# Kernel tuning notes

Hardware: AMD Instinct MI355X
Metric: run time of the kernel (lower is better)

The kernel has to match this reference:

```python
import jax, jax.numpy as jnp
import numpy as np

MUL = 32           # multiplicity of each irrep in Rs_in / Rs_out
R_EPS = 0.1        # radius below which the linear fallback kernel is used
SQRT3 = np.float32(np.sqrt(3.0))

# real-basis Levi-Civita = wigner_3j(1,1,1) * sqrt(6)
_EPS3 = np.zeros((3, 3, 3), np.float32)
_EPS3[0, 1, 2] = _EPS3[1, 2, 0] = _EPS3[2, 0, 1] = 1.0
_EPS3[0, 2, 1] = _EPS3[2, 1, 0] = _EPS3[1, 0, 2] = -1.0


def _frozen_kernel(r, W1, b1, W2, b2, lin_w0, lin_w1):
    N = r.shape[0]
    radii = jnp.linalg.norm(r, axis=1)                 # [N]
    mask = radii > R_EPS                               # [N] valid edges
    safe = jnp.where(mask, radii, jnp.ones_like(radii))
    unit = r / safe[:, None]                           # [N,3] safe unit vectors

    # radial MLP R: r -> R^(5*MUL*MUL); computed densely, masked rows replaced below
    h = jax.nn.relu(radii[:, None] * W1 + b1)          # [N,H]
    R = (h @ W2 + b2).reshape(N, 5, MUL, MUL)          # [N, path, w(out), u(in)]
    R0a, R0b, R1a, R1b, R1c = (R[:, i] for i in range(5))

    # component-normalized spherical harmonics: Y0 = 1, Y1 = sqrt(3)*unit
    Y1 = SQRT3 * unit                                  # [N,3]

    # per-path normalization: 1/sqrt(n_paths_into_output * mul_in)
    n0 = np.float32(1.0 / np.sqrt(2 * MUL))            # output l=0: 2 paths
    n1 = np.float32(1.0 / np.sqrt(3 * MUL))            # output l=1: 3 paths
    I3 = jnp.eye(3, dtype=r.dtype)
    eps3 = jnp.asarray(_EPS3, dtype=r.dtype)

    # CG tensor-product kernel blocks (w3j contracted analytically for l<=1)
    K00 = n0 * R0a                                                      # [N,w,u]
    K01 = (n0 / SQRT3) * jnp.einsum('nwu,ni->nwui', R1b, Y1)            # in l=1 -> out l=0
    K10 = n1 * jnp.einsum('nwu,nj->nwju', R1a, Y1)                      # in l=0 -> out l=1
    K11 = n1 * (jnp.einsum('nwu,ji->nwjui', R0b, I3)                    # l_f=0 path
                + np.float32(1.0 / np.sqrt(2.0))
                * jnp.einsum('nwu,nk,ikj->nwjui', R1c, Y1, eps3))       # l_f=1 path

    D = 4 * MUL  # dim = MUL*(1) + MUL*(3)
    kernel1 = jnp.zeros((N, D, D), r.dtype)
    kernel1 = kernel1.at[:, :MUL, :MUL].set(K00)
    kernel1 = kernel1.at[:, :MUL, MUL:].set(K01.reshape(N, MUL, 3 * MUL))
    kernel1 = kernel1.at[:, MUL:, :MUL].set(K10.reshape(N, 3 * MUL, MUL))
    kernel1 = kernel1.at[:, MUL:, MUL:].set(K11.reshape(N, 3 * MUL, 3 * MUL))

    # KernelLinear fallback for radii <= r_eps: block diag per l, scaled 1/sqrt(mul_in)
    s = np.float32(1.0 / np.sqrt(MUL))
    k2_11 = s * jnp.einsum('wu,ji->wjui', lin_w1, I3).reshape(3 * MUL, 3 * MUL)
    kernel2 = jnp.zeros((D, D), r.dtype)
    kernel2 = kernel2.at[:MUL, :MUL].set(s * lin_w0)
    kernel2 = kernel2.at[MUL:, MUL:].set(k2_11)

    return jnp.where(mask[:, None, None], kernel1, kernel2[None, :, :])


def setup_inputs() -> dict:
    key = jax.random.key(0)
    ks = jax.random.split(key, 6)
    N, H = 4000, 128
    r = jax.random.normal(ks[0], (N, 3), jnp.float32)
    r = r.at[:100].multiply(0.01)  # push some radii under r_eps -> fallback path
    W1 = jax.random.normal(ks[1], (1, H), jnp.float32)
    b1 = jnp.zeros((H,), jnp.float32)
    W2 = jax.random.normal(ks[2], (H, 5 * MUL * MUL), jnp.float32) / np.float32(np.sqrt(H))
    b2 = jnp.zeros((5 * MUL * MUL,), jnp.float32)
    lin_w0 = jax.random.normal(ks[3], (MUL, MUL), jnp.float32)
    lin_w1 = jax.random.normal(ks[4], (MUL, MUL), jnp.float32)
    return dict(r=r, W1=W1, b1=b1, W2=W2, b2=b2, lin_w0=lin_w0, lin_w1=lin_w1)


def reference(r, W1, b1, W2, b2, lin_w0, lin_w1):
    return _frozen_kernel(r, W1, b1, W2, b2, lin_w0, lin_w1)
```

## Files before the change

### kernel.cpp

```cpp
#include <hip/hip_runtime.h>
#include <math.h>

#define H 128
#define MUL 32
#define NC (5 * MUL * MUL)
#define DD (4 * MUL)
#define NIV (H + 1)
#define NMAX 4000

__device__ float g_bp[H];
__device__ int   g_nbp;
__device__ float g_rmid[NIV];
__device__ float g_A[NIV * NC];
__device__ float g_B[NIV * NC];
__device__ float4 g_ey[NMAX];
__device__ int    g_eidx[NMAX];

__global__ void prep_bp(const float* __restrict__ W1, const float* __restrict__ b1) {
    __shared__ float bp[H];
    __shared__ float sorted[H];
    int k = threadIdx.x;
    float a = W1[k], b = b1[k];
    float v = 3.0e38f;
    if (a != 0.0f) {
        float t = -b / a;
        if (t > 0.0f) v = t;
    }
    bp[k] = v;
    __syncthreads();
    int rank = 0, nv = 0;
    #pragma unroll 8
    for (int j = 0; j < H; ++j) {
        float bj = bp[j];
        rank += (bj < v) || (bj == v && j < k);
        nv   += (bj < 3.0e38f);
    }
    sorted[rank] = v;
    __syncthreads();
    g_bp[k] = sorted[k];
    if (k == 0) g_nbp = nv;
    int nbp = nv;
    for (int i = k; i <= H; i += H) {
        float rm;
        if (nbp == 0)       rm = 1.0f;
        else if (i == 0)    rm = 0.5f * sorted[0];
        else if (i >= nbp)  rm = sorted[nbp - 1] + 1.0f;
        else                rm = 0.5f * (sorted[i - 1] + sorted[i]);
        g_rmid[i] = rm;
    }
}

__global__ void prep_edges(const float* __restrict__ r, int N) {
    int n = blockIdx.x * blockDim.x + threadIdx.x;
    if (n >= N) return;
    float x = r[3 * n], y = r[3 * n + 1], z = r[3 * n + 2];
    float rad = sqrtf(x * x + y * y + z * z);
    bool mask = rad > 0.1f;
    float inv = mask ? (1.7320508075688772f / rad) : 0.0f;
    g_ey[n] = make_float4(x * inv, y * inv, z * inv, rad);
    int idx = -1;
    if (mask) {
        int nbp = g_nbp;
        idx = 0;
        for (int j = 0; j < nbp; ++j) idx += (g_bp[j] < rad) ? 1 : 0;
    }
    g_eidx[n] = idx;
}

__global__ __launch_bounds__(256) void prep_tab(const float* __restrict__ W1,
                                                const float* __restrict__ b1,
                                                const float* __restrict__ W2,
                                                const float* __restrict__ b2) {
    int i = blockIdx.y;
    if (i > g_nbp) return;
    int c = blockIdx.x * 256 + threadIdx.x;
    float rm = g_rmid[i];
    float accA = 0.0f, accB = 0.0f;
    #pragma unroll 4
    for (int k = 0; k < H; ++k) {
        float a = W1[k], b = b1[k];
        float w2 = W2[k * NC + c];
        bool act = (a * rm + b) > 0.0f;
        accA += act ? a * w2 : 0.0f;
        accB += act ? b * w2 : 0.0f;
    }
    g_A[i * NC + c] = accA;
    g_B[i * NC + c] = accB + b2[c];
}

__global__ __launch_bounds__(256) void main_kernel(const float* __restrict__ lin_w0,
                                                   const float* __restrict__ lin_w1,
                                                   float* __restrict__ out, int N) {
    int bid   = blockIdx.x;
    int wuBlk = bid & 15;
    int eBlk  = bid >> 4;
    int tx = threadIdx.x & 63;
    int tz = threadIdx.x >> 6;
    int n  = eBlk * 4 + tz;
    if (n >= N) return;
    int wu = wuBlk * 64 + tx;
    int w = wu >> 5, u = wu & 31;

    float* o = out + (size_t)n * (DD * DD);
    int row1 = MUL + 3 * w;
    int col1 = MUL + 3 * u;
    int idx = g_eidx[n];

    if (idx >= 0) {
        float4 ey = g_ey[n];
        float rad = ey.w;
        const float* Arow = g_A + (size_t)idx * NC;
        const float* Brow = g_B + (size_t)idx * NC;
        float acc[5];
        #pragma unroll
        for (int p = 0; p < 5; ++p) {
            int c = p * (MUL * MUL) + wu;
            acc[p] = rad * Arow[c] + Brow[c];
        }
        const float n0   = 0.125f;
        const float n1   = 0.10206207261596575f;
        const float n0s3 = 0.07216878364870323f;
        const float n1s2 = 0.07216878364870323f;
        float Y0 = ey.x, Y1 = ey.y, Y2 = ey.z;

        o[w * DD + u] = n0 * acc[0];
        float v3 = n0s3 * acc[3];
        o[w * DD + col1 + 0] = v3 * Y0;
        o[w * DD + col1 + 1] = v3 * Y1;
        o[w * DD + col1 + 2] = v3 * Y2;
        float v2 = n1 * acc[2];
        o[(row1 + 0) * DD + u] = v2 * Y0;
        o[(row1 + 1) * DD + u] = v2 * Y1;
        o[(row1 + 2) * DD + u] = v2 * Y2;
        float d = n1 * acc[1];
        float e = n1s2 * acc[4];
        float eY0 = e * Y0, eY1 = e * Y1, eY2 = e * Y2;
        o[(row1 + 0) * DD + col1 + 0] = d;
        o[(row1 + 0) * DD + col1 + 1] = eY2;
        o[(row1 + 0) * DD + col1 + 2] = -eY1;
        o[(row1 + 1) * DD + col1 + 0] = -eY2;
        o[(row1 + 1) * DD + col1 + 1] = d;
        o[(row1 + 1) * DD + col1 + 2] = eY0;
        o[(row1 + 2) * DD + col1 + 0] = eY1;
        o[(row1 + 2) * DD + col1 + 1] = -eY0;
        o[(row1 + 2) * DD + col1 + 2] = d;
    } else {
        const float s = 0.17677669529663687f;
        float v0 = s * lin_w0[w * MUL + u];
        float v1 = s * lin_w1[w * MUL + u];
        o[w * DD + u] = v0;
        o[w * DD + col1 + 0] = 0.0f;
        o[w * DD + col1 + 1] = 0.0f;
        o[w * DD + col1 + 2] = 0.0f;
        o[(row1 + 0) * DD + u] = 0.0f;
        o[(row1 + 1) * DD + u] = 0.0f;
        o[(row1 + 2) * DD + u] = 0.0f;
        o[(row1 + 0) * DD + col1 + 0] = v1;
        o[(row1 + 0) * DD + col1 + 1] = 0.0f;
        o[(row1 + 0) * DD + col1 + 2] = 0.0f;
        o[(row1 + 1) * DD + col1 + 0] = 0.0f;
        o[(row1 + 1) * DD + col1 + 1] = v1;
        o[(row1 + 1) * DD + col1 + 2] = 0.0f;
        o[(row1 + 2) * DD + col1 + 0] = 0.0f;
        o[(row1 + 2) * DD + col1 + 1] = 0.0f;
        o[(row1 + 2) * DD + col1 + 2] = v1;
    }
}

extern "C" void kernel_launch(void* const* d_in, const int* in_sizes, int n_in,
                              void* d_out, int out_size, void* d_ws, size_t ws_size,
                              hipStream_t stream) {
    const float* r   = (const float*)d_in[0];
    const float* W1  = (const float*)d_in[1];
    const float* b1  = (const float*)d_in[2];
    const float* W2  = (const float*)d_in[3];
    const float* b2  = (const float*)d_in[4];
    const float* lw0 = (const float*)d_in[5];
    const float* lw1 = (const float*)d_in[6];
    float* out = (float*)d_out;
    int N = in_sizes[0] / 3;

    prep_bp<<<dim3(1), dim3(H), 0, stream>>>(W1, b1);
    prep_edges<<<dim3((N + 255) / 256), dim3(256), 0, stream>>>(r, N);
    prep_tab<<<dim3(NC / 256, NIV), dim3(256), 0, stream>>>(W1, b1, W2, b2);
    int eChunks = (N + 3) / 4;
    main_kernel<<<dim3(eChunks * 16), dim3(256), 0, stream>>>(lw0, lw1, out, N);
}
```

Before: 68.23 us.

## Write output rows as coalesced float4 stores with one block per edge

The main kernel now assigns one block per edge and has each thread compute four consecutive output columns, writing them with a single float4 store in row-major order. Previously each thread scattered 16 scalar stores across strided rows and columns. The aim is fully coalesced, wide writes for the 256 MB output. The cost is more index arithmetic and repeated table loads, since A/B entries for the l=1 blocks are re-read for each of the three components.

```diff
diff --git a/kernel.cpp b/kernel.cpp
--- a/kernel.cpp
+++ b/kernel.cpp
@@ -15,6 +15,10 @@
 __device__ float g_B[NIV * NC];
 __device__ float4 g_ey[NMAX];
 __device__ int    g_eidx[NMAX];
+
+__device__ __forceinline__ float sel3(int i, float a, float b, float c) {
+    return (i == 0) ? a : ((i == 1) ? b : c);
+}
 
 __global__ void prep_bp(const float* __restrict__ W1, const float* __restrict__ b1) {
     __shared__ float bp[H];
@@ -91,79 +95,106 @@
 __global__ __launch_bounds__(256) void main_kernel(const float* __restrict__ lin_w0,
                                                    const float* __restrict__ lin_w1,
                                                    float* __restrict__ out, int N) {
-    int bid   = blockIdx.x;
-    int wuBlk = bid & 15;
-    int eBlk  = bid >> 4;
-    int tx = threadIdx.x & 63;
-    int tz = threadIdx.x >> 6;
-    int n  = eBlk * 4 + tz;
+    int n = blockIdx.x;
     if (n >= N) return;
-    int wu = wuBlk * 64 + tx;
-    int w = wu >> 5, u = wu & 31;
-
-    float* o = out + (size_t)n * (DD * DD);
-    int row1 = MUL + 3 * w;
-    int col1 = MUL + 3 * u;
     int idx = g_eidx[n];
+    float4* o4 = reinterpret_cast<float4*>(out + (size_t)n * (DD * DD));
+
+    const float n0   = 0.125f;
+    const float n1   = 0.10206207261596575f;
+    const float ns   = 0.07216878364870323f;
 
     if (idx >= 0) {
         float4 ey = g_ey[n];
+        float Y0 = ey.x, Y1 = ey.y, Y2 = ey.z;
         float rad = ey.w;
-        const float* Arow = g_A + (size_t)idx * NC;
-        const float* Brow = g_B + (size_t)idx * NC;
-        float acc[5];
+        const float* __restrict__ A = g_A + (size_t)idx * NC;
+        const float* __restrict__ B = g_B + (size_t)idx * NC;
+
         #pragma unroll
-        for (int p = 0; p < 5; ++p) {
-            int c = p * (MUL * MUL) + wu;
-            acc[p] = rad * Arow[c] + Brow[c];
+        for (int it = 0; it < 16; ++it) {
+            int pos  = it * 256 + threadIdx.x;
+            int row  = pos >> 5;
+            int col0 = (pos & 31) << 2;
+            float v[4];
+            if (row < MUL) {
+                int w = row;
+                if (col0 < MUL) {
+                    #pragma unroll
+                    for (int q = 0; q < 4; ++q) {
+                        int c = w * MUL + col0 + q;
+                        v[q] = n0 * (rad * A[c] + B[c]);
+                    }
+                } else {
+                    #pragma unroll
+                    for (int q = 0; q < 4; ++q) {
+                        int cc = col0 + q - MUL;
+                        int u  = (cc * 171) >> 9;
+                        int i  = cc - 3 * u;
+                        int c  = 3 * (MUL * MUL) + w * MUL + u;
+                        v[q] = ns * (rad * A[c] + B[c]) * sel3(i, Y0, Y1, Y2);
+                    }
+                }
+            } else {
+                int rr = row - MUL;
+                int w  = (rr * 171) >> 9;
+                int j  = rr - 3 * w;
+                float Yj = sel3(j, Y0, Y1, Y2);
+                int jp = (j == 2) ? 0 : (j + 1);
+                if (col0 < MUL) {
+                    #pragma unroll
+                    for (int q = 0; q < 4; ++q) {
+                        int c = 2 * (MUL * MUL) + w * MUL + col0 + q;
+                        v[q] = n1 * (rad * A[c] + B[c]) * Yj;
+                    }
+                } else {
+                    #pragma unroll
+                    for (int q = 0; q < 4; ++q) {
+                        int cc = col0 + q - MUL;
+                        int u  = (cc * 171) >> 9;
+                        int i  = cc - 3 * u;
+                        int c1 = 1 * (MUL * MUL) + w * MUL + u;
+                        int c4 = 4 * (MUL * MUL) + w * MUL + u;
+                        float rb = rad * A[c1] + B[c1];
+                        float rc = rad * A[c4] + B[c4];
+                        float Yk = sel3(3 - i - j, Y0, Y1, Y2);
+                        float sgn = (jp == i) ? 1.0f : -1.0f;
+                        v[q] = (i == j) ? (n1 * rb) : (sgn * ns * rc * Yk);
+                    }
+                }
+            }
+            o4[pos] = make_float4(v[0], v[1], v[2], v[3]);
         }
-        const float n0   = 0.125f;
-        const float n1   = 0.10206207261596575f;
-        const float n0s3 = 0.07216878364870323f;
-        const float n1s2 = 0.07216878364870323f;
-        float Y0 = ey.x, Y1 = ey.y, Y2 = ey.z;
-
-        o[w * DD + u] = n0 * acc[0];
-        float v3 = n0s3 * acc[3];
-        o[w * DD + col1 + 0] = v3 * Y0;
-        o[w * DD + col1 + 1] = v3 * Y1;
-        o[w * DD + col1 + 2] = v3 * Y2;
-        float v2 = n1 * acc[2];
-        o[(row1 + 0) * DD + u] = v2 * Y0;
-        o[(row1 + 1) * DD + u] = v2 * Y1;
-        o[(row1 + 2) * DD + u] = v2 * Y2;
-        float d = n1 * acc[1];
-        float e = n1s2 * acc[4];
-        float eY0 = e * Y0, eY1 = e * Y1, eY2 = e * Y2;
-        o[(row1 + 0) * DD + col1 + 0] = d;
-        o[(row1 + 0) * DD + col1 + 1] = eY2;
-        o[(row1 + 0) * DD + col1 + 2] = -eY1;
-        o[(row1 + 1) * DD + col1 + 0] = -eY2;
-        o[(row1 + 1) * DD + col1 + 1] = d;
-        o[(row1 + 1) * DD + col1 + 2] = eY0;
-        o[(row1 + 2) * DD + col1 + 0] = eY1;
-        o[(row1 + 2) * DD + col1 + 1] = -eY0;
-        o[(row1 + 2) * DD + col1 + 2] = d;
     } else {
         const float s = 0.17677669529663687f;
-        float v0 = s * lin_w0[w * MUL + u];
-        float v1 = s * lin_w1[w * MUL + u];
-        o[w * DD + u] = v0;
-        o[w * DD + col1 + 0] = 0.0f;
-        o[w * DD + col1 + 1] = 0.0f;
-        o[w * DD + col1 + 2] = 0.0f;
-        o[(row1 + 0) * DD + u] = 0.0f;
-        o[(row1 + 1) * DD + u] = 0.0f;
-        o[(row1 + 2) * DD + u] = 0.0f;
-        o[(row1 + 0) * DD + col1 + 0] = v1;
-        o[(row1 + 0) * DD + col1 + 1] = 0.0f;
-        o[(row1 + 0) * DD + col1 + 2] = 0.0f;
-        o[(row1 + 1) * DD + col1 + 0] = 0.0f;
-        o[(row1 + 1) * DD + col1 + 1] = v1;
-        o[(row1 + 1) * DD + col1 + 2] = 0.0f;
-        o[(row1 + 2) * DD + col1 + 0] = 0.0f;
-        o[(row1 + 2) * DD + col1 + 1] = 0.0f;
-        o[(row1 + 2) * DD + col1 + 2] = v1;
+        #pragma unroll
+        for (int it = 0; it < 16; ++it) {
+            int pos  = it * 256 + threadIdx.x;
+            int row  = pos >> 5;
+            int col0 = (pos & 31) << 2;
+            float v[4] = {0.0f, 0.0f, 0.0f, 0.0f};
+            if (row < MUL) {
+                if (col0 < MUL) {
+                    #pragma unroll
+                    for (int q = 0; q < 4; ++q)
+                        v[q] = s * lin_w0[row * MUL + col0 + q];
+                }
+            } else if (col0 >= MUL) {
+                int rr = row - MUL;
+                int w  = (rr * 171) >> 9;
+                int j  = rr - 3 * w;
+                float lw = s * lin_w1[w * MUL + 0];
+                (void)lw;
+                #pragma unroll
+                for (int q = 0; q < 4; ++q) {
+                    int cc = col0 + q - MUL;
+                    int u  = (cc * 171) >> 9;
+                    int i  = cc - 3 * u;
+                    v[q] = (i == j) ? s * lin_w1[w * MUL + u] : 0.0f;
+                }
+            }
+            o4[pos] = make_float4(v[0], v[1], v[2], v[3]);
+        }
     }
 }
 
@@ -183,6 +214,5 @@
     prep_bp<<<dim3(1), dim3(H), 0, stream>>>(W1, b1);
     prep_edges<<<dim3((N + 255) / 256), dim3(256), 0, stream>>>(r, N);
     prep_tab<<<dim3(NC / 256, NIV), dim3(256), 0, stream>>>(W1, b1, W2, b2);
-    int eChunks = (N + 3) / 4;
-    main_kernel<<<dim3(eChunks * 16), dim3(256), 0, stream>>>(lw0, lw1, out, N);
-}
+    main_kernel<<<dim3(N), dim3(256), 0, stream>>>(lw0, lw1, out, N);
+}
```

New measurement: 152.9 us. 124% more time.
